# Kernel tuning notes

Hardware: AMD Instinct MI355X
Metric: run time of the kernel (lower is better)

## Reference

```python
import jax, jax.numpy as jnp
import numpy as np

B, L = 2, 256
H, W = 256, 128
FLAT = H * W              # 32768
D_MODEL = 1024
D_INNER = 2 * D_MODEL     # 2048
D_STATE = 16
D_CONV = 4
DT_RANK = D_MODEL // 16   # 64


def _rmsnorm(x, w, eps=1e-5):
    return x * jax.lax.rsqrt(jnp.mean(x * x, axis=-1, keepdims=True) + eps) * w


def _selective_scan(dA, dBu, C):
    # dA, dBu: (B, L, D_INNER, D_STATE); C: (B, L, D_STATE)
    def step(h, inp):
        a, bu, c = inp
        h = a * h + bu
        return h, jnp.einsum('bdn,bn->bd', h, c)
    h0 = jnp.zeros((dA.shape[0], dA.shape[2], dA.shape[3]), dA.dtype)
    _, ys = jax.lax.scan(step, h0, (jnp.swapaxes(dA, 0, 1), jnp.swapaxes(dBu, 0, 1), jnp.swapaxes(C, 0, 1)))
    return jnp.swapaxes(ys, 0, 1)  # (B, L, D_INNER)


def _mamba_block(x, norm_w, in_proj_w, conv_w, conv_b, x_proj_w, dt_proj_w, dt_proj_b, A_log, D_skip, out_proj_w):
    xn = _rmsnorm(x, norm_w)
    xz = xn @ in_proj_w.T                        # (B, L, 2*D_INNER)
    u, z = jnp.split(xz, 2, axis=-1)
    # causal depthwise conv over the sequence dim
    u = jax.lax.conv_general_dilated(u, conv_w, (1,), [(D_CONV - 1, 0)],
                                     dimension_numbers=('NWC', 'WIO', 'NWC'),
                                     feature_group_count=D_INNER) + conv_b
    u = jax.nn.silu(u)
    dbc = u @ x_proj_w.T                         # (B, L, DT_RANK + 2*D_STATE)
    dt_r, Bm, Cm = jnp.split(dbc, [DT_RANK, DT_RANK + D_STATE], axis=-1)
    dt = jax.nn.softplus(dt_r @ dt_proj_w.T + dt_proj_b)  # (B, L, D_INNER)
    A = -jnp.exp(A_log)                          # (D_INNER, D_STATE)
    dA = jnp.exp(dt[..., None] * A)              # (B, L, D_INNER, D_STATE)
    dBu = (dt * u)[..., None] * Bm[:, :, None, :]
    y = _selective_scan(dA, dBu, Cm) + D_skip * u
    y = y * jax.nn.silu(z)
    return x + y @ out_proj_w.T


def setup_inputs():
    key = jax.random.key(0)
    ks = jax.random.split(key, 12)
    g = lambda i, shape, sc: jax.random.normal(ks[i], shape, dtype=jnp.float32) * sc
    return {
        'x': (jax.random.uniform(ks[0], (B, L, H, W)) < 0.1).astype(jnp.float32),
        'enc_w': g(1, (D_MODEL, FLAT), 0.005),
        'enc_b': jnp.zeros((D_MODEL,), jnp.float32),
        'dec_w': g(2, (FLAT, D_MODEL), 0.02),
        'dec_b': jnp.zeros((FLAT,), jnp.float32),
        'norm_w': jnp.ones((D_MODEL,), jnp.float32),
        'in_proj_w': g(3, (2 * D_INNER, D_MODEL), 0.02),
        'conv_w': g(4, (D_CONV, 1, D_INNER), 0.2),
        'conv_b': jnp.zeros((D_INNER,), jnp.float32),
        'x_proj_w': g(5, (DT_RANK + 2 * D_STATE, D_INNER), 0.02),
        'dt_proj_w': g(6, (D_INNER, DT_RANK), 0.1),
        'dt_proj_b': jnp.full((D_INNER,), -2.0, jnp.float32),
        'A_log': jnp.log(jnp.tile(jnp.arange(1, D_STATE + 1, dtype=jnp.float32), (D_INNER, 1))),
        'D_skip': jnp.ones((D_INNER,), jnp.float32),
        'out_proj_w': g(7, (D_MODEL, D_INNER), 0.02),
    }


def reference(x, enc_w, enc_b, dec_w, dec_b, norm_w, in_proj_w, conv_w, conv_b,
              x_proj_w, dt_proj_w, dt_proj_b, A_log, D_skip, out_proj_w):
    b, l = x.shape[:2]
    lat = x.reshape(b, l, FLAT) @ enc_w.T + enc_b          # frozen encoder
    h = _mamba_block(lat, norm_w, in_proj_w, conv_w, conv_b, x_proj_w,
                     dt_proj_w, dt_proj_b, A_log, D_skip, out_proj_w)
    probs = jax.nn.sigmoid(h @ dec_w.T + dec_b)            # frozen decoder + sigmoid
    return probs.reshape(b, l, H, W)[:, :-1]
```

## Files before the change

kernel.cpp:

```cpp
#include <hip/hip_runtime.h>
#include <math.h>
#include <stdint.h>

#define BB 2
#define LL 256
#define FLAT 32768
#define DM 1024
#define DI 2048
#define DS 16
#define DTR 64
#define ML (BB*LL)

#define EPI_NONE 0
#define EPI_BIAS 1
#define EPI_SOFTPLUS 2
#define EPI_DEC 4

typedef __attribute__((ext_vector_type(8))) short bf16x8;
typedef __attribute__((ext_vector_type(4))) float f32x4;
typedef __attribute__((ext_vector_type(8))) unsigned short u16x8;
typedef __attribute__((ext_vector_type(4))) unsigned short u16x4;

__device__ __forceinline__ float sigmoid_f(float x) { return 1.0f / (1.0f + __expf(-x)); }

__device__ __forceinline__ unsigned short f2bf(float f) {
    unsigned u = __float_as_uint(f);
    u += 0x7fffu + ((u >> 16) & 1u);
    return (unsigned short)(u >> 16);
}

__device__ __forceinline__ unsigned cvt_pk_bf16(float a, float b) {
    unsigned r;
    asm("v_cvt_pk_bf16_f32 %0, %1, %2" : "=v"(r) : "v"(a), "v"(b));
    return r;
}

__device__ __forceinline__ void gld_lds16(const void* g, void* l) {
    __builtin_amdgcn_global_load_lds(
        (const __attribute__((address_space(1))) unsigned int*)g,
        (__attribute__((address_space(3))) unsigned int*)l, 16, 0, 0);
}

__global__ __launch_bounds__(256) void cvt_bf16_k(
    const float* __restrict__ in, unsigned short* __restrict__ out, int n8)
{
    const int i = blockIdx.x * 256 + threadIdx.x;
    if (i >= n8) return;
    const float4 a = ((const float4*)in)[2 * i];
    const float4 b = ((const float4*)in)[2 * i + 1];
    u16x8 r;
    r[0] = f2bf(a.x); r[1] = f2bf(a.y); r[2] = f2bf(a.z); r[3] = f2bf(a.w);
    r[4] = f2bf(b.x); r[5] = f2bf(b.y); r[6] = f2bf(b.z); r[7] = f2bf(b.w);
    ((u16x8*)out)[i] = r;
}

template<int EPI, bool SPLIT, bool BF32>
__global__ __launch_bounds__(256) void gemm_bf16(
    const unsigned short* __restrict__ A, const void* __restrict__ Bv,
    float* __restrict__ C, int M, int N, int K, int lda, int ldb, int kChunk,
    const float* __restrict__ bias)
{
    __shared__ __align__(16) char lds[BF32 ? 49152 : 32768];

    const float*          Bf = (const float*)Bv;
    const unsigned short* Bh = (const unsigned short*)Bv;

    const int t  = threadIdx.x;
    const int w  = t >> 6;
    const int l  = t & 63;
    const int m0 = blockIdx.x * 128;
    const int n0 = blockIdx.y * 128;
    const int wr = w >> 1, wc = w & 1;

    int kb = 0, ke = K;
    float* Cout = C;
    if (SPLIT) { kb = blockIdx.z * kChunk; ke = kb + kChunk;
                 Cout = C + (size_t)blockIdx.z * M * N; }

    const int srow0 = w * 32 + (l >> 3);
    const int ssub  = l & 7;
    const int brow0 = w * 32 + (l >> 4);
    const int bgl   = l & 15;

    f32x4 acc[4][4];
#pragma unroll
    for (int i = 0; i < 4; ++i)
#pragma unroll
        for (int j = 0; j < 4; ++j) acc[i][j] = (f32x4){0.f, 0.f, 0.f, 0.f};

    const int lr = l & 15, h = l >> 4;

    for (int kt = kb; kt < ke; kt += 64) {
#pragma unroll
        for (int q = 0; q < 4; ++q) {
            const int row = srow0 + q * 8;
            gld_lds16(A + (size_t)(m0 + row) * lda + kt + ((ssub ^ (row & 7)) << 3),
                      lds + w * 4096 + q * 1024);
        }
        if (BF32) {
#pragma unroll
            for (int q = 0; q < 8; ++q) {
                const int row = brow0 + q * 4;
                gld_lds16(Bf + (size_t)(n0 + row) * ldb + kt + ((bgl ^ (row & 15)) << 2),
                          lds + 16384 + w * 8192 + q * 1024);
            }
        } else {
#pragma unroll
            for (int q = 0; q < 4; ++q) {
                const int row = srow0 + q * 8;
                gld_lds16(Bh + (size_t)(n0 + row) * ldb + kt + ((ssub ^ (row & 7)) << 3),
                          lds + 16384 + w * 4096 + q * 1024);
            }
        }
        __syncthreads();

#pragma unroll
        for (int ks = 0; ks < 2; ++ks) {
            bf16x8 af[4], bfr[4];
#pragma unroll
            for (int i = 0; i < 4; ++i) {
                const int r = wr * 64 + i * 16 + lr;
                const int sub = (ks * 4 + h) ^ (r & 7);
                af[i] = *(const bf16x8*)(lds + r * 128 + sub * 16);
            }
#pragma unroll
            for (int j = 0; j < 4; ++j) {
                const int c = wc * 64 + j * 16 + lr;
                if (BF32) {
                    const int g0 = (2 * (ks * 4 + h))     ^ (c & 15);
                    const int g1 = (2 * (ks * 4 + h) + 1) ^ (c & 15);
                    const f32x4 v0 = *(const f32x4*)(lds + 16384 + c * 256 + g0 * 16);
                    const f32x4 v1 = *(const f32x4*)(lds + 16384 + c * 256 + g1 * 16);
                    union { unsigned u[4]; bf16x8 v; } cv;
                    cv.u[0] = cvt_pk_bf16(v0[0], v0[1]);
                    cv.u[1] = cvt_pk_bf16(v0[2], v0[3]);
                    cv.u[2] = cvt_pk_bf16(v1[0], v1[1]);
                    cv.u[3] = cvt_pk_bf16(v1[2], v1[3]);
                    bfr[j] = cv.v;
                } else {
                    const int sub = (ks * 4 + h) ^ (c & 7);
                    bfr[j] = *(const bf16x8*)(lds + 16384 + c * 128 + sub * 16);
                }
            }
#pragma unroll
            for (int i = 0; i < 4; ++i)
#pragma unroll
                for (int j = 0; j < 4; ++j)
                    acc[i][j] = __builtin_amdgcn_mfma_f32_16x16x32_bf16(
                        af[i], bfr[j], acc[i][j], 0, 0, 0);
        }
        __syncthreads();
    }

#pragma unroll
    for (int i = 0; i < 4; ++i)
#pragma unroll
        for (int j = 0; j < 4; ++j)
#pragma unroll
            for (int rg = 0; rg < 4; ++rg) {
                const int row = m0 + wr * 64 + i * 16 + h * 4 + rg;
                const int col = n0 + wc * 64 + j * 16 + lr;
                float v = acc[i][j][rg];
                if (SPLIT || EPI == EPI_NONE) {
                    Cout[(size_t)row * N + col] = v;
                } else if (EPI == EPI_DEC) {
                    v = sigmoid_f(v + bias[col]);
                    const int b = row >> 8, ll = row & 255;
                    if (ll < 255) Cout[(((size_t)(b * 255 + ll)) << 15) + col] = v;
                }
            }
}

template<int EPI, bool SPLIT>
__global__ __launch_bounds__(256) void gemm_nt(
    const float* __restrict__ A, const float* __restrict__ B,
    float* __restrict__ C, int M, int N, int K, int lda, int ldb,
    int kChunk, const float* __restrict__ bias)
{
    __shared__ float As[32][64];
    __shared__ float Bs[32][64];

    const int m0 = blockIdx.x * 64;
    const int n0 = blockIdx.y * 64;
    const int t  = threadIdx.x;

    int kb = 0, ke = K;
    float* Cout = C;
    if (SPLIT) { kb = blockIdx.z * kChunk; ke = kb + kChunk; Cout = C + (size_t)blockIdx.z * M * N; }

    const int lrow = t >> 3;
    const int lcol = (t & 7) << 2;

    float acc[4][4];
#pragma unroll
    for (int i = 0; i < 4; ++i)
#pragma unroll
        for (int j = 0; j < 4; ++j) acc[i][j] = 0.0f;

    const int tx = t & 15, ty = t >> 4;

    for (int k = kb; k < ke; k += 32) {
#pragma unroll
        for (int i = 0; i < 2; ++i) {
            const int row = lrow + i * 32;
            float4 av = *(const float4*)&A[(m0 + row) * lda + k + lcol];
            As[lcol + 0][row] = av.x; As[lcol + 1][row] = av.y;
            As[lcol + 2][row] = av.z; As[lcol + 3][row] = av.w;
            const int nn = n0 + row;
            float4 bv = make_float4(0.f, 0.f, 0.f, 0.f);
            if (nn < N) bv = *(const float4*)&B[nn * ldb + k + lcol];
            Bs[lcol + 0][row] = bv.x; Bs[lcol + 1][row] = bv.y;
            Bs[lcol + 2][row] = bv.z; Bs[lcol + 3][row] = bv.w;
        }
        __syncthreads();
#pragma unroll
        for (int kk = 0; kk < 32; ++kk) {
            float4 a4 = *(const float4*)&As[kk][ty << 2];
            float4 b4 = *(const float4*)&Bs[kk][tx << 2];
            const float a[4] = { a4.x, a4.y, a4.z, a4.w };
            const float b[4] = { b4.x, b4.y, b4.z, b4.w };
#pragma unroll
            for (int i = 0; i < 4; ++i)
#pragma unroll
                for (int j = 0; j < 4; ++j)
                    acc[i][j] = fmaf(a[i], b[j], acc[i][j]);
        }
        __syncthreads();
    }

#pragma unroll
    for (int i = 0; i < 4; ++i) {
        const int m = m0 + (ty << 2) + i;
#pragma unroll
        for (int j = 0; j < 4; ++j) {
            const int n = n0 + (tx << 2) + j;
            if (n >= N) continue;
            float v = acc[i][j];
            if (SPLIT || EPI == EPI_NONE) {
                Cout[m * N + n] = v;
            } else if (EPI == EPI_SOFTPLUS) {
                v += bias[n];
                Cout[m * N + n] = fmaxf(v, 0.0f) + log1pf(__expf(-fabsf(v)));
            }
        }
    }
}

template<int EPI>
__global__ __launch_bounds__(256) void splitk_reduce(
    const float* __restrict__ part, float* __restrict__ C,
    int MN, int N, int S, const float* __restrict__ bias)
{
    const int i = blockIdx.x * 256 + threadIdx.x;
    if (i >= MN) return;
    float s = 0.0f;
    for (int j = 0; j < S; ++j) s += part[(size_t)j * MN + i];
    if (EPI == EPI_BIAS) s += bias[i % N];
    C[i] = s;
}

__global__ __launch_bounds__(256) void splitk_reduce_resid_bf16(
    const float* __restrict__ part, const float* __restrict__ resid,
    unsigned short* __restrict__ outb, int MN, int S)
{
    const int i = blockIdx.x * 256 + threadIdx.x;
    if (i >= MN) return;
    float s = 0.0f;
    for (int j = 0; j < S; ++j) s += part[(size_t)j * MN + i];
    outb[i] = f2bf(s + resid[i]);
}

__global__ __launch_bounds__(256) void rmsnorm_k(
    const float* __restrict__ x, const float* __restrict__ w,
    unsigned short* __restrict__ o)
{
    const int row = blockIdx.x;
    const int t = threadIdx.x;
    const float* xr = x + row * DM;
    float4 xv = *(const float4*)&xr[t * 4];
    float ss = xv.x * xv.x + xv.y * xv.y + xv.z * xv.z + xv.w * xv.w;
#pragma unroll
    for (int off = 32; off > 0; off >>= 1) ss += __shfl_xor(ss, off);
    __shared__ float red[4];
    if ((t & 63) == 0) red[t >> 6] = ss;
    __syncthreads();
    const float tot = red[0] + red[1] + red[2] + red[3];
    const float scale = rsqrtf(tot * (1.0f / DM) + 1e-5f);
    float4 wv = *(const float4*)&w[t * 4];
    u16x4 ov;
    ov[0] = f2bf(xv.x * scale * wv.x); ov[1] = f2bf(xv.y * scale * wv.y);
    ov[2] = f2bf(xv.z * scale * wv.z); ov[3] = f2bf(xv.w * scale * wv.w);
    *(u16x4*)&o[row * DM + t * 4] = ov;
}

__global__ __launch_bounds__(256) void conv_silu_k(
    const float* __restrict__ xz, const float* __restrict__ cw,
    const float* __restrict__ cb, float* __restrict__ u)
{
    const int idx = blockIdx.x * 256 + threadIdx.x;
    if (idx >= ML * DI) return;
    const int d  = idx & (DI - 1);
    const int bl = idx >> 11;
    const int l  = bl & (LL - 1);
    float s = cb[d];
#pragma unroll
    for (int w = 0; w < 4; ++w) {
        const int ls = l - 3 + w;
        if (ls >= 0) s = fmaf(xz[(bl - 3 + w) * (2 * DI) + d], cw[w * DI + d], s);
    }
    u[idx] = s * sigmoid_f(s);
}

__global__ __launch_bounds__(256) void scan_k(
    const float* __restrict__ dt, const float* __restrict__ u,
    const float* __restrict__ xz, const float* __restrict__ dbc,
    const float* __restrict__ A_log, const float* __restrict__ Dskip,
    unsigned short* __restrict__ y)
{
    const int t = blockIdx.x * 256 + threadIdx.x;
    const int n  = t & (DS - 1);
    const int ch = t >> 4;
    const int d  = ch & (DI - 1);
    const int b  = ch >> 11;
    const float a  = -__expf(A_log[d * DS + n]);
    const float Dv = Dskip[d];
    float h = 0.0f;
    const int rbase = b * LL;

    for (int l0 = 0; l0 < LL; l0 += 8) {
        float dtv[8], uv[8], Bv[8], Cv[8], zv[8];
#pragma unroll
        for (int s = 0; s < 8; ++s) {
            const int r = rbase + l0 + s;
            dtv[s] = dt[r * DI + d];
            uv[s]  = u[r * DI + d];
            Bv[s]  = dbc[r * 96 + DTR + n];
            Cv[s]  = dbc[r * 96 + DTR + DS + n];
            zv[s]  = xz[r * (2 * DI) + DI + d];
        }
        float p[8];
#pragma unroll
        for (int s = 0; s < 8; ++s) {
            const float dA = __expf(dtv[s] * a);
            h = fmaf(dA, h, dtv[s] * uv[s] * Bv[s]);
            p[s] = h * Cv[s];
        }
#pragma unroll
        for (int s = 0; s < 8; ++s) p[s] += __shfl_xor(p[s], 1);
#pragma unroll
        for (int s = 0; s < 8; ++s) p[s] += __shfl_xor(p[s], 2);
#pragma unroll
        for (int s = 0; s < 8; ++s) p[s] += __shfl_xor(p[s], 4);
#pragma unroll
        for (int s = 0; s < 8; ++s) p[s] += __shfl_xor(p[s], 8);
        if (n == 0) {
#pragma unroll
            for (int s = 0; s < 8; ++s) {
                const int r = rbase + l0 + s;
                const float yy = fmaf(Dv, uv[s], p[s]);
                y[r * DI + d] = f2bf(yy * zv[s] * sigmoid_f(zv[s]));
            }
        }
    }
}

extern "C" void kernel_launch(void* const* d_in, const int* in_sizes, int n_in,
                              void* d_out, int out_size, void* d_ws, size_t ws_size,
                              hipStream_t stream)
{
    const float* x        = (const float*)d_in[0];
    const float* enc_w    = (const float*)d_in[1];
    const float* enc_b    = (const float*)d_in[2];
    const float* dec_w    = (const float*)d_in[3];
    const float* dec_b    = (const float*)d_in[4];
    const float* norm_w   = (const float*)d_in[5];
    const float* in_proj  = (const float*)d_in[6];
    const float* conv_w   = (const float*)d_in[7];
    const float* conv_b   = (const float*)d_in[8];
    const float* x_proj   = (const float*)d_in[9];
    const float* dt_projw = (const float*)d_in[10];
    const float* dt_projb = (const float*)d_in[11];
    const float* A_log    = (const float*)d_in[12];
    const float* D_skip   = (const float*)d_in[13];
    const float* out_proj = (const float*)d_in[14];
    float* out = (float*)d_out;
    (void)in_sizes; (void)n_in; (void)out_size; (void)ws_size;

    char* wsb = (char*)d_ws;
    float* part = (float*)(wsb);
    float* lat  = (float*)(wsb + 67108864);
    float* dt   = (float*)(wsb + 69206016);
    char* S0 = wsb + 73400320;
    unsigned short* xbf    = (unsigned short*)(S0);
    unsigned short* xnbf   = (unsigned short*)(S0);
    unsigned short* ybf    = (unsigned short*)(S0 + 1048576);
    unsigned short* houtbf = (unsigned short*)(S0 + 3145728);
    float* xz  = (float*)(S0 + 4194304);
    float* u   = (float*)(S0 + 12582912);
    float* dbc = (float*)(S0 + 16777216);

    cvt_bf16_k<<<(FLAT * ML / 8) / 256, 256, 0, stream>>>(x, xbf, FLAT * ML / 8);

    {
        dim3 g(ML / 128, DM / 128, 32);
        gemm_bf16<EPI_NONE, true, true><<<g, 256, 0, stream>>>(
            xbf, enc_w, part, ML, DM, FLAT, FLAT, FLAT, FLAT / 32, nullptr);
        splitk_reduce<EPI_BIAS><<<(ML * DM) / 256, 256, 0, stream>>>(part, lat, ML * DM, DM, 32, enc_b);
    }

    rmsnorm_k<<<ML, 256, 0, stream>>>(lat, norm_w, xnbf);

    {
        dim3 g(ML / 128, (2 * DI) / 128);
        gemm_bf16<EPI_NONE, false, true><<<g, 256, 0, stream>>>(
            xnbf, in_proj, xz, ML, 2 * DI, DM, DM, DM, 0, nullptr);
    }

    conv_silu_k<<<(ML * DI) / 256, 256, 0, stream>>>(xz, conv_w, conv_b, u);

    {
        dim3 g(ML / 64, 2, 16);
        gemm_nt<EPI_NONE, true><<<g, 256, 0, stream>>>(u, x_proj, part, ML, 96, DI, DI, DI,
                                                       DI / 16, nullptr);
        splitk_reduce<EPI_NONE><<<(ML * 96 + 255) / 256, 256, 0, stream>>>(part, dbc, ML * 96, 96, 16, nullptr);
    }

    {
        dim3 g(ML / 64, DI / 64);
        gemm_nt<EPI_SOFTPLUS, false><<<g, 256, 0, stream>>>(dbc, dt_projw, dt, ML, DI, DTR,
                                                            96, DTR, 0, dt_projb);
    }

    scan_k<<<(BB * DI * DS) / 256, 256, 0, stream>>>(dt, u, xz, dbc, A_log, D_skip, ybf);

    {
        dim3 g(ML / 128, DM / 128, 8);
        gemm_bf16<EPI_NONE, true, true><<<g, 256, 0, stream>>>(
            ybf, out_proj, part, ML, DM, DI, DI, DI, DI / 8, nullptr);
        splitk_reduce_resid_bf16<<<(ML * DM) / 256, 256, 0, stream>>>(part, lat, houtbf, ML * DM, 8);
    }

    {
        dim3 g(ML / 128, FLAT / 128);
        gemm_bf16<EPI_DEC, false, true><<<g, 256, 0, stream>>>(
            houtbf, dec_w, out, ML, FLAT, DM, DM, DM, 0, dec_b);
    }
}
```

Baseline: 634.6 us.

## Pre-convert encoder/decoder weights to bf16 and use double-buffered async-LDS GEMM

Adds a GEMM kernel that takes bf16 operands for both A and B, stages tiles straight into LDS with a swizzle, and double-buffers so the next K tile loads while MFMAs run on the current one. The fp32 encoder and decoder weights are converted to bf16 in a separate pass each call, and the encoder split-K factor drops from 32 to 16. This trades an extra full read and write of two large weight matrices for cheaper, better-overlapped GEMM inner loops. It also needs a larger workspace.

```diff
diff --git a/kernel.cpp b/kernel.cpp
--- a/kernel.cpp
+++ b/kernel.cpp
@@ -52,6 +52,108 @@
     r[0] = f2bf(a.x); r[1] = f2bf(a.y); r[2] = f2bf(a.z); r[3] = f2bf(a.w);
     r[4] = f2bf(b.x); r[5] = f2bf(b.y); r[6] = f2bf(b.z); r[7] = f2bf(b.w);
     ((u16x8*)out)[i] = r;
+}
+
+template<int EPI, bool SPLIT>
+__global__ __launch_bounds__(256) void gemm_db(
+    const unsigned short* __restrict__ A, const unsigned short* __restrict__ B,
+    float* __restrict__ C, int M, int N, int K, int lda, int ldb, int kChunk,
+    const float* __restrict__ bias)
+{
+    __shared__ __align__(16) char lds[65536];
+
+    const int t  = threadIdx.x;
+    const int w  = t >> 6;
+    const int l  = t & 63;
+    const int m0 = blockIdx.x * 128;
+    const int n0 = blockIdx.y * 128;
+    const int wr = w >> 1, wc = w & 1;
+
+    int kb = 0, ke = K;
+    float* Cout = C;
+    if (SPLIT) { kb = blockIdx.z * kChunk; ke = kb + kChunk;
+                 Cout = C + (size_t)blockIdx.z * M * N; }
+
+    const int srow0 = w * 32 + (l >> 3);
+    const int ssub  = l & 7;
+
+    f32x4 acc[4][4];
+#pragma unroll
+    for (int i = 0; i < 4; ++i)
+#pragma unroll
+        for (int j = 0; j < 4; ++j) acc[i][j] = (f32x4){0.f, 0.f, 0.f, 0.f};
+
+    const int lr = l & 15, h = l >> 4;
+
+    auto STAGE = [&](int p, int kt) {
+#pragma unroll
+        for (int q = 0; q < 4; ++q) {
+            const int row = srow0 + q * 8;
+            gld_lds16(A + (size_t)(m0 + row) * lda + kt + ((ssub ^ (row & 7)) << 3),
+                      lds + p * 32768 + w * 4096 + q * 1024);
+        }
+#pragma unroll
+        for (int q = 0; q < 4; ++q) {
+            const int row = srow0 + q * 8;
+            gld_lds16(B + (size_t)(n0 + row) * ldb + kt + ((ssub ^ (row & 7)) << 3),
+                      lds + p * 32768 + 16384 + w * 4096 + q * 1024);
+        }
+    };
+
+    STAGE(0, kb);
+    asm volatile("s_waitcnt vmcnt(0)" ::: "memory");
+    __builtin_amdgcn_s_barrier();
+
+    const int nt = (ke - kb) >> 6;
+    int cur = 0;
+    for (int tt = 0; tt < nt; ++tt) {
+        if (tt + 1 < nt) STAGE(cur ^ 1, kb + ((tt + 1) << 6));
+        const char* la = lds + cur * 32768;
+        const char* lb = la + 16384;
+#pragma unroll
+        for (int ks = 0; ks < 2; ++ks) {
+            bf16x8 af[4], bfr[4];
+#pragma unroll
+            for (int i = 0; i < 4; ++i) {
+                const int r = wr * 64 + i * 16 + lr;
+                const int sub = (ks * 4 + h) ^ (r & 7);
+                af[i] = *(const bf16x8*)(la + r * 128 + sub * 16);
+            }
+#pragma unroll
+            for (int j = 0; j < 4; ++j) {
+                const int c = wc * 64 + j * 16 + lr;
+                const int sub = (ks * 4 + h) ^ (c & 7);
+                bfr[j] = *(const bf16x8*)(lb + c * 128 + sub * 16);
+            }
+#pragma unroll
+            for (int i = 0; i < 4; ++i)
+#pragma unroll
+                for (int j = 0; j < 4; ++j)
+                    acc[i][j] = __builtin_amdgcn_mfma_f32_16x16x32_bf16(
+                        af[i], bfr[j], acc[i][j], 0, 0, 0);
+        }
+        asm volatile("s_waitcnt vmcnt(0)" ::: "memory");
+        __builtin_amdgcn_s_barrier();
+        cur ^= 1;
+    }
+
+#pragma unroll
+    for (int i = 0; i < 4; ++i)
+#pragma unroll
+        for (int j = 0; j < 4; ++j)
+#pragma unroll
+            for (int rg = 0; rg < 4; ++rg) {
+                const int row = m0 + wr * 64 + i * 16 + h * 4 + rg;
+                const int col = n0 + wc * 64 + j * 16 + lr;
+                float v = acc[i][j][rg];
+                if (SPLIT || EPI == EPI_NONE) {
+                    Cout[(size_t)row * N + col] = v;
+                } else if (EPI == EPI_DEC) {
+                    v = sigmoid_f(v + bias[col]);
+                    const int b = row >> 8, ll = row & 255;
+                    if (ll < 255) Cout[(((size_t)(b * 255 + ll)) << 15) + col] = v;
+                }
+            }
 }
 
 template<int EPI, bool SPLIT, bool BF32>
@@ -387,10 +489,11 @@
     (void)in_sizes; (void)n_in; (void)out_size; (void)ws_size;
 
     char* wsb = (char*)d_ws;
-    float* part = (float*)(wsb);
-    float* lat  = (float*)(wsb + 67108864);
-    float* dt   = (float*)(wsb + 69206016);
-    char* S0 = wsb + 73400320;
+    unsigned short* wbf = (unsigned short*)(wsb);
+    float* part = (float*)(wsb + 67108864);
+    float* lat  = (float*)(wsb + 100663296);
+    float* dt   = (float*)(wsb + 102760448);
+    char* S0 = wsb + 106954752;
     unsigned short* xbf    = (unsigned short*)(S0);
     unsigned short* xnbf   = (unsigned short*)(S0);
     unsigned short* ybf    = (unsigned short*)(S0 + 1048576);
@@ -400,12 +503,13 @@
     float* dbc = (float*)(S0 + 16777216);
 
     cvt_bf16_k<<<(FLAT * ML / 8) / 256, 256, 0, stream>>>(x, xbf, FLAT * ML / 8);
+    cvt_bf16_k<<<(DM * FLAT / 8) / 256, 256, 0, stream>>>(enc_w, wbf, DM * FLAT / 8);
 
     {
-        dim3 g(ML / 128, DM / 128, 32);
-        gemm_bf16<EPI_NONE, true, true><<<g, 256, 0, stream>>>(
-            xbf, enc_w, part, ML, DM, FLAT, FLAT, FLAT, FLAT / 32, nullptr);
-        splitk_reduce<EPI_BIAS><<<(ML * DM) / 256, 256, 0, stream>>>(part, lat, ML * DM, DM, 32, enc_b);
+        dim3 g(ML / 128, DM / 128, 16);
+        gemm_db<EPI_NONE, true><<<g, 256, 0, stream>>>(
+            xbf, wbf, part, ML, DM, FLAT, FLAT, FLAT, FLAT / 16, nullptr);
+        splitk_reduce<EPI_BIAS><<<(ML * DM) / 256, 256, 0, stream>>>(part, lat, ML * DM, DM, 16, enc_b);
     }
 
     rmsnorm_k<<<ML, 256, 0, stream>>>(lat, norm_w, xnbf);
@@ -440,9 +544,10 @@
         splitk_reduce_resid_bf16<<<(ML * DM) / 256, 256, 0, stream>>>(part, lat, houtbf, ML * DM, 8);
     }
 
+    cvt_bf16_k<<<(FLAT * DM / 8) / 256, 256, 0, stream>>>(dec_w, wbf, FLAT * DM / 8);
     {
         dim3 g(ML / 128, FLAT / 128);
-        gemm_bf16<EPI_DEC, false, true><<<g, 256, 0, stream>>>(
-            houtbf, dec_w, out, ML, FLAT, DM, DM, DM, 0, dec_b);
-    }
-}
+        gemm_db<EPI_DEC, false><<<g, 256, 0, stream>>>(
+            houtbf, wbf, out, ML, FLAT, DM, DM, DM, 0, dec_b);
+    }
+}
```

Result: no change. 633.5 us (-0.2%).
